# Optimization experiments

Measured on AMD Instinct MI355X. Metric: run time of the kernel, lower is better.

Reference implementation:

```python
import jax, jax.numpy as jnp
import numpy as np

N_NODES = 50000
N_EDGES = 800000
IN_CH = 128
HID = 64
N_LAYERS = 14
EPS_MSG = 1e-7
EPS_SM = 1e-16
LN_EPS = 1e-5


def setup_inputs() -> dict:
    key = jax.random.key(0)
    ks = jax.random.split(key, 8)
    x = jax.random.normal(ks[0], (N_NODES, IN_CH), dtype=jnp.float32)
    edge_index = jax.random.randint(ks[1], (2, N_EDGES), 0, N_NODES, dtype=jnp.int64)
    enc_W = jax.random.normal(ks[2], (IN_CH, HID), dtype=jnp.float32) / np.sqrt(IN_CH)
    enc_b = jnp.zeros((HID,), dtype=jnp.float32)
    mlp_W = jax.random.normal(ks[3], (N_LAYERS, HID, HID), dtype=jnp.float32) / np.sqrt(HID)
    mlp_b = jnp.zeros((N_LAYERS, HID), dtype=jnp.float32)
    t = jnp.ones((N_LAYERS,), dtype=jnp.float32)  # learn_t, init t=1.0
    return {"x": x, "edge_index": edge_index, "enc_W": enc_W, "enc_b": enc_b,
            "mlp_W": mlp_W, "mlp_b": mlp_b, "t": t}


def _layernorm(h):
    # LayerNorm(elementwise_affine=False) over last dim
    mu = jnp.mean(h, axis=-1, keepdims=True)
    var = jnp.mean((h - mu) ** 2, axis=-1, keepdims=True)
    return (h - mu) * jax.lax.rsqrt(var + LN_EPS)


def _segment_softmax(scores, seg, num_segments):
    # per-target-node, per-channel softmax over incoming edges
    m = jax.ops.segment_max(scores, seg, num_segments=num_segments)
    e = jnp.exp(scores - m[seg])
    s = jax.ops.segment_sum(e, seg, num_segments=num_segments)
    return e / (s[seg] + EPS_SM)


def _genconv(h, src, dst, W, b, t):
    # GENConv: msg = relu(x_j) + eps; softmax_sg aggregation (weights detached);
    # out = MLP(aggr + x) where MLP is a single Linear
    msg = jax.nn.relu(h[src]) + EPS_MSG                       # [E, H]
    alpha = _segment_softmax(t * msg, dst, N_NODES)           # [E, H]
    alpha = jax.lax.stop_gradient(alpha)                      # 'softmax_sg'
    aggr = jax.ops.segment_sum(msg * alpha, dst, num_segments=N_NODES)
    return (aggr + h) @ W + b


def reference(x, edge_index, enc_W, enc_b, mlp_W, mlp_b, t):
    src, dst = edge_index[0], edge_index[1]
    h = x @ enc_W + enc_b                                     # node encoder
    h = _genconv(h, src, dst, mlp_W[0], mlp_b[0], t[0])       # layers[0].conv

    def body(carry, params):
        W, b, tt = params
        y = jax.nn.relu(_layernorm(carry))                    # res+ pre-norm/act
        y = _genconv(y, src, dst, W, b, tt)                   # dropout inactive (eval)
        return carry + y, None

    h, _ = jax.lax.scan(body, h, (mlp_W[1:], mlp_b[1:], t[1:]))
    h = jax.nn.relu(_layernorm(h))                            # final norm + act
    return jax.nn.log_softmax(h, axis=-1)
```

## Files before the change

### kernel.cpp

```cpp
#include <hip/hip_runtime.h>

#define NN 50000
#define NE 800000
#define INC 128
#define HIDC 64
#define NL 14
#define EPS_MSG 1e-7f
#define EPS_SM 1e-16f
#define LN_EPS 1e-5f
#define LOG2E 1.44269504088896f

#define SCAN_B 256
#define NB_SCAN ((NN + SCAN_B - 1) / SCAN_B)

__device__ __forceinline__ float wave_sum(float v) {
    #pragma unroll
    for (int o = 32; o > 0; o >>= 1) v += __shfl_xor(v, o, 64);
    return v;
}
__device__ __forceinline__ float wave_max(float v) {
    #pragma unroll
    for (int o = 32; o > 0; o >>= 1) v = fmaxf(v, __shfl_xor(v, o, 64));
    return v;
}
__device__ __forceinline__ float bcast(float x, int l) {
    return __int_as_float(__builtin_amdgcn_readlane(__float_as_int(x), l));
}
__device__ __forceinline__ float fexp2(float x) {
    float r; asm("v_exp_f32 %0, %1" : "=v"(r) : "v"(x)); return r;
}
__device__ __forceinline__ unsigned pack_bf2(float lo, float hi) {
    unsigned ul = __float_as_uint(lo); ul += 0x7fffu + ((ul >> 16) & 1u);
    unsigned uh = __float_as_uint(hi); uh += 0x7fffu + ((uh >> 16) & 1u);
    return (ul >> 16) | (uh & 0xffff0000u);
}

__global__ void k_hist(const int* __restrict__ dst, int* __restrict__ deg) {
    int i = blockIdx.x * blockDim.x + threadIdx.x;
    if (i < NE) atomicAdd(&deg[dst[i]], 1);
}

__global__ void k_part(const int* __restrict__ deg, int* __restrict__ part) {
    __shared__ int sm[SCAN_B];
    int b = blockIdx.x;
    int i = b * SCAN_B + threadIdx.x;
    sm[threadIdx.x] = (i < NN) ? deg[i] : 0;
    __syncthreads();
    for (int s = SCAN_B / 2; s > 0; s >>= 1) {
        if (threadIdx.x < s) sm[threadIdx.x] += sm[threadIdx.x + s];
        __syncthreads();
    }
    if (threadIdx.x == 0) part[b] = sm[0];
}

__global__ void k_scanpart(const int* __restrict__ part, int* __restrict__ partOfs) {
    __shared__ int sm[SCAN_B];
    int t = threadIdx.x;
    int own = (t < NB_SCAN) ? part[t] : 0;
    sm[t] = own;
    __syncthreads();
    for (int o = 1; o < SCAN_B; o <<= 1) {
        int v = (t >= o) ? sm[t - o] : 0;
        __syncthreads();
        sm[t] += v;
        __syncthreads();
    }
    if (t < NB_SCAN) partOfs[t] = sm[t] - own;
}

__global__ void k_scanfinal(const int* __restrict__ deg, const int* __restrict__ partOfs,
                            int* __restrict__ rowOfs) {
    __shared__ int sm[SCAN_B];
    int b = blockIdx.x, t = threadIdx.x;
    int i = b * SCAN_B + t;
    int d = (i < NN) ? deg[i] : 0;
    sm[t] = d;
    __syncthreads();
    for (int o = 1; o < SCAN_B; o <<= 1) {
        int v = (t >= o) ? sm[t - o] : 0;
        __syncthreads();
        sm[t] += v;
        __syncthreads();
    }
    if (i < NN) rowOfs[i] = partOfs[b] + sm[t] - d;
    if (i == 0) rowOfs[NN] = NE;
}

__global__ void k_scatter(const int* __restrict__ src, const int* __restrict__ dst,
                          int* __restrict__ rowCur, int* __restrict__ csrB) {
    int i = blockIdx.x * blockDim.x + threadIdx.x;
    if (i < NE) {
        int p = atomicAdd(&rowCur[dst[i]], 1);
        csrB[p] = src[i] << 7;
    }
}

__global__ __launch_bounds__(256) void k_enc(const float* __restrict__ x,
                                             const float* __restrict__ W,
                                             const float* __restrict__ bias,
                                             const float* __restrict__ tptr,
                                             float* __restrict__ h,
                                             unsigned* __restrict__ B0) {
    __shared__ float XL[32 * INC];
    __shared__ float WL[INC * HIDC];
    int tid = threadIdx.x;
    for (int i = tid; i < (INC * HIDC) / 4; i += 256)
        ((float4*)WL)[i] = ((const float4*)W)[i];
    int r0 = blockIdx.x * 32;
    for (int i = tid; i < (32 * INC) / 4; i += 256) {
        int row = i >> 5;
        float4 val = make_float4(0.f, 0.f, 0.f, 0.f);
        if (r0 + row < NN) val = ((const float4*)x)[(size_t)(r0 + row) * 32 + (i & 31)];
        ((float4*)XL)[i] = val;
    }
    __syncthreads();
    int lane = tid & 63, w = tid >> 6;
    float bv = bias[lane];
    float sc = tptr[0] * LOG2E;
    #pragma unroll
    for (int i = 0; i < 4; i++) {
        int ra = w * 8 + i * 2, rb = ra + 1;
        float a0 = 0.f, a1 = 0.f, a2 = 0.f, a3 = 0.f;
        float c0 = 0.f, c1 = 0.f, c2 = 0.f, c3 = 0.f;
        #pragma unroll
        for (int k = 0; k < INC; k += 4) {
            float4 xa = *(const float4*)&XL[ra * INC + k];
            float4 xb = *(const float4*)&XL[rb * INC + k];
            float w0 = WL[(k + 0) * HIDC + lane];
            float w1 = WL[(k + 1) * HIDC + lane];
            float w2 = WL[(k + 2) * HIDC + lane];
            float w3 = WL[(k + 3) * HIDC + lane];
            a0 = fmaf(xa.x, w0, a0); a1 = fmaf(xa.y, w1, a1);
            a2 = fmaf(xa.z, w2, a2); a3 = fmaf(xa.w, w3, a3);
            c0 = fmaf(xb.x, w0, c0); c1 = fmaf(xb.y, w1, c1);
            c2 = fmaf(xb.z, w2, c2); c3 = fmaf(xb.w, w3, c3);
        }
        int ga = r0 + ra, gb = r0 + rb;
        float va = bv + ((a0 + a1) + (a2 + a3));
        float vb = bv + ((c0 + c1) + (c2 + c3));
        float sa = sc * fmaxf(va, 0.f), sb = sc * fmaxf(vb, 0.f);
        float pa = __shfl_xor(sa, 1, 64);
        float pb = __shfl_xor(sb, 1, 64);
        if (ga < NN) {
            h[(size_t)ga * HIDC + lane] = va;
            if (!(lane & 1)) B0[(size_t)ga * 32 + (lane >> 1)] = pack_bf2(sa, pa);
        }
        if (gb < NN) {
            h[(size_t)gb * HIDC + lane] = vb;
            if (!(lane & 1)) B0[(size_t)gb * 32 + (lane >> 1)] = pack_bf2(sb, pb);
        }
    }
}

template<bool FIRST>
__global__ __launch_bounds__(256) void k_aggr(const float* __restrict__ henc,
                                              const unsigned* __restrict__ Bin,
                                              const int* __restrict__ rowOfs,
                                              const int* __restrict__ csrB,
                                              const float* __restrict__ tptr,
                                              float* __restrict__ A) {
    int lane = threadIdx.x & 63;
    int v = (blockIdx.x * 256 + threadIdx.x) >> 6;
    int g = lane >> 4;
    int c = lane & 15;
    const char* basec = (const char*)Bin + (c << 3);
    float invs = 1.0f / (tptr[0] * LOG2E);

    int e0 = rowOfs[v], e1 = rowOfs[v + 1];
    float se0 = 0.f, se1 = 0.f, se2 = 0.f, se3 = 0.f;
    float sw0 = 0.f, sw1 = 0.f, sw2 = 0.f, sw3 = 0.f;
    int e = e0;
    for (; e + 16 <= e1; e += 16) {
        #pragma unroll
        for (int j = 0; j < 4; j++) {
            int off = csrB[e + 4 * j + g];
            uint2 q = *(const uint2*)(basec + off);
            float g0 = __uint_as_float(q.x << 16);
            float g1 = __uint_as_float(q.x & 0xffff0000u);
            float g2 = __uint_as_float(q.y << 16);
            float g3 = __uint_as_float(q.y & 0xffff0000u);
            float w0 = fexp2(g0), w1 = fexp2(g1), w2 = fexp2(g2), w3 = fexp2(g3);
            se0 += w0; sw0 = fmaf(g0, w0, sw0);
            se1 += w1; sw1 = fmaf(g1, w1, sw1);
            se2 += w2; sw2 = fmaf(g2, w2, sw2);
            se3 += w3; sw3 = fmaf(g3, w3, sw3);
        }
    }
    if (e < e1) {
        #pragma unroll
        for (int j = 0; j < 4; j++) {
            int ee = e + 4 * j + g;
            bool valid = ee < e1;
            int off = csrB[valid ? ee : e0];
            uint2 q = *(const uint2*)(basec + off);
            float g0 = __uint_as_float(q.x << 16);
            float g1 = __uint_as_float(q.x & 0xffff0000u);
            float g2 = __uint_as_float(q.y << 16);
            float g3 = __uint_as_float(q.y & 0xffff0000u);
            float w0 = valid ? fexp2(g0) : 0.f;
            float w1 = valid ? fexp2(g1) : 0.f;
            float w2 = valid ? fexp2(g2) : 0.f;
            float w3 = valid ? fexp2(g3) : 0.f;
            se0 += w0; sw0 = fmaf(g0, w0, sw0);
            se1 += w1; sw1 = fmaf(g1, w1, sw1);
            se2 += w2; sw2 = fmaf(g2, w2, sw2);
            se3 += w3; sw3 = fmaf(g3, w3, sw3);
        }
    }
    #pragma unroll
    for (int m = 16; m <= 32; m <<= 1) {
        se0 += __shfl_xor(se0, m, 64); sw0 += __shfl_xor(sw0, m, 64);
        se1 += __shfl_xor(se1, m, 64); sw1 += __shfl_xor(sw1, m, 64);
        se2 += __shfl_xor(se2, m, 64); sw2 += __shfl_xor(sw2, m, 64);
        se3 += __shfl_xor(se3, m, 64); sw3 += __shfl_xor(sw3, m, 64);
    }
    if (g == 0) {
        float4 r;
        r.x = sw0 / (se0 + EPS_SM) * invs + EPS_MSG;
        r.y = sw1 / (se1 + EPS_SM) * invs + EPS_MSG;
        r.z = sw2 / (se2 + EPS_SM) * invs + EPS_MSG;
        r.w = sw3 / (se3 + EPS_SM) * invs + EPS_MSG;
        if (FIRST) {
            float4 s4 = ((const float4*)henc)[(size_t)v * 16 + c];
            r.x += s4.x; r.y += s4.y; r.z += s4.z; r.w += s4.w;
        }
        ((float4*)A)[(size_t)v * 16 + c] = r;
    }
}

template<bool LNRES, int MODE>
__global__ __launch_bounds__(256) void k_mlp(const float* __restrict__ A,
                                             float* __restrict__ h,
                                             unsigned* __restrict__ Bout,
                                             const float* __restrict__ W,
                                             const float* __restrict__ b,
                                             const float* __restrict__ tnext) {
    __shared__ float WL[HIDC * HIDC];
    for (int i = threadIdx.x; i < (HIDC * HIDC) / 4; i += 256)
        ((float4*)WL)[i] = ((const float4*)W)[i];
    __syncthreads();

    int lane = threadIdx.x & 63;
    int wid = (blockIdx.x * 256 + threadIdx.x) >> 6;
    int nw = (gridDim.x * 256) >> 6;
    float bv = b[lane];
    float sc = (MODE == 0) ? tnext[0] * LOG2E : 0.f;

    for (int v = wid; v < NN; v += nw) {
        float a = A[(size_t)v * HIDC + lane];
        float base = bv;
        if (LNRES) {
            float hv = h[(size_t)v * HIDC + lane];
            float mu = wave_sum(hv) * (1.f / 64.f);
            float d = hv - mu;
            float var = wave_sum(d * d) * (1.f / 64.f);
            a += fmaxf(d * rsqrtf(var + LN_EPS), 0.f);
            base += hv;
        }
        float a0 = 0.f, a1 = 0.f, a2 = 0.f, a3 = 0.f;
        #pragma unroll
        for (int k = 0; k < 64; k += 4) {
            a0 = fmaf(bcast(a, k + 0), WL[(k + 0) * HIDC + lane], a0);
            a1 = fmaf(bcast(a, k + 1), WL[(k + 1) * HIDC + lane], a1);
            a2 = fmaf(bcast(a, k + 2), WL[(k + 2) * HIDC + lane], a2);
            a3 = fmaf(bcast(a, k + 3), WL[(k + 3) * HIDC + lane], a3);
        }
        float acc = base + ((a0 + a1) + (a2 + a3));

        if (MODE == 1) {
            float mu = wave_sum(acc) * (1.f / 64.f);
            float d = acc - mu;
            float var = wave_sum(d * d) * (1.f / 64.f);
            float z = fmaxf(d * rsqrtf(var + LN_EPS), 0.f);
            float m = wave_max(z);
            float s2 = wave_sum(fexp2((z - m) * LOG2E));
            h[(size_t)v * HIDC + lane] = z - (m + __logf(s2));
        } else {
            h[(size_t)v * HIDC + lane] = acc;
            float mu = wave_sum(acc) * (1.f / 64.f);
            float d = acc - mu;
            float var = wave_sum(d * d) * (1.f / 64.f);
            float y = sc * fmaxf(d * rsqrtf(var + LN_EPS), 0.f);
            float yp = __shfl_xor(y, 1, 64);
            if (!(lane & 1)) Bout[(size_t)v * 32 + (lane >> 1)] = pack_bf2(y, yp);
        }
    }
}

extern "C" void kernel_launch(void* const* d_in, const int* in_sizes, int n_in,
                              void* d_out, int out_size, void* d_ws, size_t ws_size,
                              hipStream_t stream) {
    const float* x    = (const float*)d_in[0];
    const int*   ei   = (const int*)d_in[1];
    const float* encW = (const float*)d_in[2];
    const float* encb = (const float*)d_in[3];
    const float* mlpW = (const float*)d_in[4];
    const float* mlpb = (const float*)d_in[5];
    const float* t    = (const float*)d_in[6];

    float* h = (float*)d_out;

    char* ws = (char*)d_ws;
    size_t off = 0;
    auto alloc = [&](size_t bytes) -> void* {
        void* p = ws + off;
        off += (bytes + 255) / 256 * 256;
        return p;
    };
    float*    henc   = (float*)alloc((size_t)NN * HIDC * 4);
    float*    A      = (float*)alloc((size_t)NN * HIDC * 4);
    unsigned* B0     = (unsigned*)alloc((size_t)NN * 32 * 4);
    unsigned* B1     = (unsigned*)alloc((size_t)NN * 32 * 4);
    int*      deg    = (int*)alloc((size_t)NN * 4);
    int*      rowOfs = (int*)alloc((size_t)(NN + 1) * 4);
    int*      rowCur = (int*)alloc((size_t)NN * 4);
    int*      part   = (int*)alloc((size_t)NB_SCAN * 4);
    int*      partOf = (int*)alloc((size_t)NB_SCAN * 4);
    int*      csrB   = (int*)alloc((size_t)NE * 4);

    const int* src = ei;
    const int* dst = ei + NE;

    hipMemsetAsync(deg, 0, (size_t)NN * 4, stream);

    k_hist<<<(NE + 255) / 256, 256, 0, stream>>>(dst, deg);
    k_part<<<NB_SCAN, SCAN_B, 0, stream>>>(deg, part);
    k_scanpart<<<1, SCAN_B, 0, stream>>>(part, partOf);
    k_scanfinal<<<NB_SCAN, SCAN_B, 0, stream>>>(deg, partOf, rowOfs);
    hipMemcpyAsync(rowCur, rowOfs, (size_t)NN * 4, hipMemcpyDeviceToDevice, stream);
    k_scatter<<<(NE + 255) / 256, 256, 0, stream>>>(src, dst, rowCur, csrB);

    k_enc<<<(NN + 31) / 32, 256, 0, stream>>>(x, encW, encb, t, henc, B0);

    k_aggr<true><<<12500, 256, 0, stream>>>(henc, B0, rowOfs, csrB, t, A);
    k_mlp<false, 0><<<2048, 256, 0, stream>>>(A, h, B1, mlpW, mlpb, t + 1);

    for (int l = 1; l < NL - 1; l++) {
        unsigned* Bi = (l & 1) ? B1 : B0;
        unsigned* Bo = (l & 1) ? B0 : B1;
        k_aggr<false><<<12500, 256, 0, stream>>>(nullptr, Bi, rowOfs, csrB, t + l, A);
        k_mlp<true, 0><<<2048, 256, 0, stream>>>(A, h, Bo,
                                                 mlpW + (size_t)l * HIDC * HIDC,
                                                 mlpb + (size_t)l * HIDC, t + l + 1);
    }
    k_aggr<false><<<12500, 256, 0, stream>>>(nullptr, B1, rowOfs, csrB, t + (NL - 1), A);
    k_mlp<true, 1><<<2048, 256, 0, stream>>>(A, h, nullptr,
                                             mlpW + (size_t)(NL - 1) * HIDC * HIDC,
                                             mlpb + (size_t)(NL - 1) * HIDC, nullptr);
}
```

Measured before the change: 1.030 ms.

## Split bf16 feature buffer into channel-half planes and use 16-bit CSR indices

The packed bf16 node features are stored as two planes, one per 32-channel half. The aggregation grid is doubled so each wave gathers a single 64-byte half-row per edge for one plane, which shrinks the randomly accessed working set per plane so it is more likely to stay in cache. CSR source indices are now stored as 16-bit node ids, which works because there are fewer than 65536 nodes, and this halves the index traffic. The rowCur copy is folded into the scan kernel, removing a separate memcpy. In exchange, every edge index is read twice, once per plane, and the kernel runs twice as many waves, each doing more shuffle reduction steps.

```diff
diff --git a/kernel.cpp b/kernel.cpp
--- a/kernel.cpp
+++ b/kernel.cpp
@@ -69,7 +69,7 @@
 }
 
 __global__ void k_scanfinal(const int* __restrict__ deg, const int* __restrict__ partOfs,
-                            int* __restrict__ rowOfs) {
+                            int* __restrict__ rowOfs, int* __restrict__ rowCur) {
     __shared__ int sm[SCAN_B];
     int b = blockIdx.x, t = threadIdx.x;
     int i = b * SCAN_B + t;
@@ -82,16 +82,20 @@
         sm[t] += v;
         __syncthreads();
     }
-    if (i < NN) rowOfs[i] = partOfs[b] + sm[t] - d;
+    if (i < NN) {
+        int r = partOfs[b] + sm[t] - d;
+        rowOfs[i] = r;
+        rowCur[i] = r;
+    }
     if (i == 0) rowOfs[NN] = NE;
 }
 
 __global__ void k_scatter(const int* __restrict__ src, const int* __restrict__ dst,
-                          int* __restrict__ rowCur, int* __restrict__ csrB) {
+                          int* __restrict__ rowCur, unsigned short* __restrict__ csrU) {
     int i = blockIdx.x * blockDim.x + threadIdx.x;
     if (i < NE) {
         int p = atomicAdd(&rowCur[dst[i]], 1);
-        csrB[p] = src[i] << 7;
+        csrU[p] = (unsigned short)src[i];
     }
 }
 
@@ -115,6 +119,7 @@
     }
     __syncthreads();
     int lane = tid & 63, w = tid >> 6;
+    int pl = lane >> 5, wd = (lane & 31) >> 1;
     float bv = bias[lane];
     float sc = tptr[0] * LOG2E;
     #pragma unroll
@@ -143,11 +148,11 @@
         float pb = __shfl_xor(sb, 1, 64);
         if (ga < NN) {
             h[(size_t)ga * HIDC + lane] = va;
-            if (!(lane & 1)) B0[(size_t)ga * 32 + (lane >> 1)] = pack_bf2(sa, pa);
+            if (!(lane & 1)) B0[((size_t)pl * NN + ga) * 16 + wd] = pack_bf2(sa, pa);
         }
         if (gb < NN) {
             h[(size_t)gb * HIDC + lane] = vb;
-            if (!(lane & 1)) B0[(size_t)gb * 32 + (lane >> 1)] = pack_bf2(sb, pb);
+            if (!(lane & 1)) B0[((size_t)pl * NN + gb) * 16 + wd] = pack_bf2(sb, pb);
         }
     }
 }
@@ -156,14 +161,16 @@
 __global__ __launch_bounds__(256) void k_aggr(const float* __restrict__ henc,
                                               const unsigned* __restrict__ Bin,
                                               const int* __restrict__ rowOfs,
-                                              const int* __restrict__ csrB,
+                                              const unsigned short* __restrict__ csrU,
                                               const float* __restrict__ tptr,
                                               float* __restrict__ A) {
     int lane = threadIdx.x & 63;
-    int v = (blockIdx.x * 256 + threadIdx.x) >> 6;
-    int g = lane >> 4;
-    int c = lane & 15;
-    const char* basec = (const char*)Bin + (c << 3);
+    int wid = (blockIdx.x * 256 + threadIdx.x) >> 6;
+    int p = (wid >= NN) ? 1 : 0;
+    int v = wid - p * NN;
+    int g = lane >> 3;
+    int c = lane & 7;
+    const char* basec = (const char*)Bin + (((size_t)p * NN) << 6) + (c << 3);
     float invs = 1.0f / (tptr[0] * LOG2E);
 
     int e0 = rowOfs[v], e1 = rowOfs[v + 1];
@@ -172,8 +179,8 @@
     int e = e0;
     for (; e + 16 <= e1; e += 16) {
         #pragma unroll
-        for (int j = 0; j < 4; j++) {
-            int off = csrB[e + 4 * j + g];
+        for (int j = 0; j < 2; j++) {
+            int off = (int)csrU[e + 8 * j + g] << 6;
             uint2 q = *(const uint2*)(basec + off);
             float g0 = __uint_as_float(q.x << 16);
             float g1 = __uint_as_float(q.x & 0xffff0000u);
@@ -188,10 +195,10 @@
     }
     if (e < e1) {
         #pragma unroll
-        for (int j = 0; j < 4; j++) {
-            int ee = e + 4 * j + g;
+        for (int j = 0; j < 2; j++) {
+            int ee = e + 8 * j + g;
             bool valid = ee < e1;
-            int off = csrB[valid ? ee : e0];
+            int off = (int)csrU[valid ? ee : e0] << 6;
             uint2 q = *(const uint2*)(basec + off);
             float g0 = __uint_as_float(q.x << 16);
             float g1 = __uint_as_float(q.x & 0xffff0000u);
@@ -208,7 +215,7 @@
         }
     }
     #pragma unroll
-    for (int m = 16; m <= 32; m <<= 1) {
+    for (int m = 8; m <= 32; m <<= 1) {
         se0 += __shfl_xor(se0, m, 64); sw0 += __shfl_xor(sw0, m, 64);
         se1 += __shfl_xor(se1, m, 64); sw1 += __shfl_xor(sw1, m, 64);
         se2 += __shfl_xor(se2, m, 64); sw2 += __shfl_xor(sw2, m, 64);
@@ -221,10 +228,10 @@
         r.z = sw2 / (se2 + EPS_SM) * invs + EPS_MSG;
         r.w = sw3 / (se3 + EPS_SM) * invs + EPS_MSG;
         if (FIRST) {
-            float4 s4 = ((const float4*)henc)[(size_t)v * 16 + c];
+            float4 s4 = ((const float4*)henc)[(size_t)v * 16 + p * 8 + c];
             r.x += s4.x; r.y += s4.y; r.z += s4.z; r.w += s4.w;
         }
-        ((float4*)A)[(size_t)v * 16 + c] = r;
+        ((float4*)A)[(size_t)v * 16 + p * 8 + c] = r;
     }
 }
 
@@ -243,6 +250,7 @@
     int lane = threadIdx.x & 63;
     int wid = (blockIdx.x * 256 + threadIdx.x) >> 6;
     int nw = (gridDim.x * 256) >> 6;
+    int pl = lane >> 5, wd = (lane & 31) >> 1;
     float bv = b[lane];
     float sc = (MODE == 0) ? tnext[0] * LOG2E : 0.f;
 
@@ -282,7 +290,7 @@
             float var = wave_sum(d * d) * (1.f / 64.f);
             float y = sc * fmaxf(d * rsqrtf(var + LN_EPS), 0.f);
             float yp = __shfl_xor(y, 1, 64);
-            if (!(lane & 1)) Bout[(size_t)v * 32 + (lane >> 1)] = pack_bf2(y, yp);
+            if (!(lane & 1)) Bout[((size_t)pl * NN + v) * 16 + wd] = pack_bf2(y, yp);
         }
     }
 }
@@ -307,16 +315,16 @@
         off += (bytes + 255) / 256 * 256;
         return p;
     };
-    float*    henc   = (float*)alloc((size_t)NN * HIDC * 4);
-    float*    A      = (float*)alloc((size_t)NN * HIDC * 4);
-    unsigned* B0     = (unsigned*)alloc((size_t)NN * 32 * 4);
-    unsigned* B1     = (unsigned*)alloc((size_t)NN * 32 * 4);
-    int*      deg    = (int*)alloc((size_t)NN * 4);
-    int*      rowOfs = (int*)alloc((size_t)(NN + 1) * 4);
-    int*      rowCur = (int*)alloc((size_t)NN * 4);
-    int*      part   = (int*)alloc((size_t)NB_SCAN * 4);
-    int*      partOf = (int*)alloc((size_t)NB_SCAN * 4);
-    int*      csrB   = (int*)alloc((size_t)NE * 4);
+    float*          henc   = (float*)alloc((size_t)NN * HIDC * 4);
+    float*          A      = (float*)alloc((size_t)NN * HIDC * 4);
+    unsigned*       B0     = (unsigned*)alloc((size_t)NN * 32 * 4);
+    unsigned*       B1     = (unsigned*)alloc((size_t)NN * 32 * 4);
+    int*            deg    = (int*)alloc((size_t)NN * 4);
+    int*            rowOfs = (int*)alloc((size_t)(NN + 1) * 4);
+    int*            rowCur = (int*)alloc((size_t)NN * 4);
+    int*            part   = (int*)alloc((size_t)NB_SCAN * 4);
+    int*            partOf = (int*)alloc((size_t)NB_SCAN * 4);
+    unsigned short* csrU   = (unsigned short*)alloc((size_t)NE * 2);
 
     const int* src = ei;
     const int* dst = ei + NE;
@@ -326,24 +334,23 @@
     k_hist<<<(NE + 255) / 256, 256, 0, stream>>>(dst, deg);
     k_part<<<NB_SCAN, SCAN_B, 0, stream>>>(deg, part);
     k_scanpart<<<1, SCAN_B, 0, stream>>>(part, partOf);
-    k_scanfinal<<<NB_SCAN, SCAN_B, 0, stream>>>(deg, partOf, rowOfs);
-    hipMemcpyAsync(rowCur, rowOfs, (size_t)NN * 4, hipMemcpyDeviceToDevice, stream);
-    k_scatter<<<(NE + 255) / 256, 256, 0, stream>>>(src, dst, rowCur, csrB);
+    k_scanfinal<<<NB_SCAN, SCAN_B, 0, stream>>>(deg, partOf, rowOfs, rowCur);
+    k_scatter<<<(NE + 255) / 256, 256, 0, stream>>>(src, dst, rowCur, csrU);
 
     k_enc<<<(NN + 31) / 32, 256, 0, stream>>>(x, encW, encb, t, henc, B0);
 
-    k_aggr<true><<<12500, 256, 0, stream>>>(henc, B0, rowOfs, csrB, t, A);
+    k_aggr<true><<<25000, 256, 0, stream>>>(henc, B0, rowOfs, csrU, t, A);
     k_mlp<false, 0><<<2048, 256, 0, stream>>>(A, h, B1, mlpW, mlpb, t + 1);
 
     for (int l = 1; l < NL - 1; l++) {
         unsigned* Bi = (l & 1) ? B1 : B0;
         unsigned* Bo = (l & 1) ? B0 : B1;
-        k_aggr<false><<<12500, 256, 0, stream>>>(nullptr, Bi, rowOfs, csrB, t + l, A);
+        k_aggr<false><<<25000, 256, 0, stream>>>(nullptr, Bi, rowOfs, csrU, t + l, A);
         k_mlp<true, 0><<<2048, 256, 0, stream>>>(A, h, Bo,
                                                  mlpW + (size_t)l * HIDC * HIDC,
                                                  mlpb + (size_t)l * HIDC, t + l + 1);
     }
-    k_aggr<false><<<12500, 256, 0, stream>>>(nullptr, B1, rowOfs, csrB, t + (NL - 1), A);
+    k_aggr<false><<<25000, 256, 0, stream>>>(nullptr, B1, rowOfs, csrU, t + (NL - 1), A);
     k_mlp<true, 1><<<2048, 256, 0, stream>>>(A, h, nullptr,
                                              mlpW + (size_t)(NL - 1) * HIDC * HIDC,
                                              mlpb + (size_t)(NL - 1) * HIDC, nullptr);
```

New measurement: 1.133 ms. +10.0%, slower.
